# Optimization experiments

Measured on AMD Instinct MI355X. Metric: run time of the kernel, lower is better.

The kernel has to match this reference:

```python
import jax, jax.numpy as jnp
import numpy as np

B, L, HID, NH = 4, 1024, 768, 12
HD = HID // NH  # head dim 64
VOCAB, MPE = 30, 2048
NW, WL = 8, 16
BETA = 1.0


def setup_inputs() -> dict:
    key = jax.random.key(0)
    ks = jax.random.split(key, 10)
    hidden_states = jax.random.normal(ks[0], (B, L, HID), dtype=jnp.float32)
    attention_mask = jnp.zeros((B, 1, 1, L), dtype=jnp.float32)
    distance = jax.random.randint(ks[1], (B, L, L), 0, 1022, dtype=jnp.int32)
    random_walk = jax.random.randint(ks[2], (B, L, NW, WL), 0, VOCAB, dtype=jnp.int32)
    anonymous_random_walk = jax.random.randint(ks[3], (B, L, NW, WL), 0, VOCAB, dtype=jnp.int32)
    s = 0.02
    Wq = jax.random.normal(ks[4], (HID, HID), dtype=jnp.float32) * s
    Wk = jax.random.normal(ks[5], (HID, HID), dtype=jnp.float32) * s
    Wv = jax.random.normal(ks[6], (HID, HID), dtype=jnp.float32) * s
    bq = jnp.zeros((HID,), jnp.float32)
    bk = jnp.zeros((HID,), jnp.float32)
    bv = jnp.zeros((HID,), jnp.float32)
    node_emb = jax.random.normal(ks[7], (VOCAB, HID), dtype=jnp.float32) * s
    node_emb = node_emb.at[0].set(0.0)  # padding_idx=0
    dist_emb = jax.random.normal(ks[8], (MPE, NH), dtype=jnp.float32) * s
    dist_emb = dist_emb.at[0].set(0.0)  # padding_idx=0
    return dict(hidden_states=hidden_states, attention_mask=attention_mask,
                Wq=Wq, bq=bq, Wk=Wk, bk=bk, Wv=Wv, bv=bv,
                node_emb=node_emb, dist_emb=dist_emb,
                distance=distance, random_walk=random_walk,
                anonymous_random_walk=anonymous_random_walk)


def _heads(x):  # [B,L,HID] -> [B,NH,L,HD]
    return x.reshape(B, L, NH, HD).transpose(0, 2, 1, 3)


def _walk_bias(walk, node_emb):
    # walk: [B,L,NW,WL] int -> embed [B,L,NW,WL,HID] -> sum dims (2,3) -> [B,L,HID]
    pe = jnp.sum(node_emb[walk], axis=(2, 3))
    e = _heads(pe)  # [B,NH,L,HD]
    return jnp.einsum('bhid,bhjd->bhij', e, e)


def reference(hidden_states, attention_mask, Wq, bq, Wk, bk, Wv, bv,
              node_emb, dist_emb, distance, random_walk, anonymous_random_walk):
    q = _heads(hidden_states @ Wq.T + bq)
    k = _heads(hidden_states @ Wk.T + bk)
    v = _heads(hidden_states @ Wv.T + bv)
    scores = jnp.einsum('bhid,bhjd->bhij', q, k) / np.sqrt(HD).astype(np.float32)
    # distance RPE: [B,L,L,NH] -> [B,NH,L,L]
    bias = dist_emb[distance + 1].transpose(0, 3, 1, 2)
    bias = bias + _walk_bias(random_walk, node_emb)
    bias = bias + _walk_bias(anonymous_random_walk, node_emb)
    scores = scores + bias * BETA + attention_mask
    probs = jax.nn.softmax(scores, axis=-1)
    ctx = jnp.einsum('bhij,bhjd->bhid', probs, v)
    return ctx.transpose(0, 2, 1, 3).reshape(B, L, HID)
```

## Files before the change

### kernel.cpp

```cpp
#include <hip/hip_runtime.h>
#include <hip/hip_bf16.h>

#define LL 1024
#define HID 768
#define NH 12
#define HD 64
#define KAUG 192
#define NBH 48

typedef unsigned int u32;
typedef unsigned short u16;
typedef __bf16 bf16_t;
typedef bf16_t bf16x8 __attribute__((ext_vector_type(8)));
typedef _Float16 f16x4 __attribute__((ext_vector_type(4)));
typedef float f32x4 __attribute__((ext_vector_type(4)));
typedef u32 u32x4 __attribute__((ext_vector_type(4)));

__device__ __forceinline__ u16 f2b(float f) {
    union { float f; u32 u; } v; v.f = f;
    u32 r = v.u + 0x7fffu + ((v.u >> 16) & 1u);
    return (u16)(r >> 16);
}
__device__ __forceinline__ u16 f2h(float f) {
    _Float16 h = (_Float16)f;
    return __builtin_bit_cast(u16, h);
}
__device__ __forceinline__ float h2f(u16 v) {
    return (float)__builtin_bit_cast(_Float16, v);
}
__device__ __forceinline__ bf16x8 load8s(const u16* p) {
    return __builtin_bit_cast(bf16x8, *reinterpret_cast<const u32x4*>(p));
}
__device__ __forceinline__ f16x4 load4h(const u16* p) {
    return __builtin_bit_cast(f16x4, *reinterpret_cast<const unsigned long long*>(p));
}
__device__ __forceinline__ void cvt4_store_v(u16* dst, float4 f) {
    ushort4 o;
    o.x = f2b(f.x); o.y = f2b(f.y); o.z = f2b(f.z); o.w = f2b(f.w);
    *reinterpret_cast<ushort4*>(dst) = o;
}

__global__ __launch_bounds__(256) void k_pack(const int* __restrict__ distance, u16* __restrict__ distu) {
    int idx = (blockIdx.x * 256 + threadIdx.x) * 8;
    int4 a = *reinterpret_cast<const int4*>(&distance[idx]);
    int4 b = *reinterpret_cast<const int4*>(&distance[idx + 4]);
    u32x4 w;
    w[0] = (u32)(u16)(a.x + 1) | ((u32)(u16)(a.y + 1) << 16);
    w[1] = (u32)(u16)(a.z + 1) | ((u32)(u16)(a.w + 1) << 16);
    w[2] = (u32)(u16)(b.x + 1) | ((u32)(u16)(b.y + 1) << 16);
    w[3] = (u32)(u16)(b.z + 1) | ((u32)(u16)(b.w + 1) << 16);
    *reinterpret_cast<u32x4*>(&distu[idx]) = w;
}

__global__ __launch_bounds__(256) void k_qkv(const float* __restrict__ hs,
                                             const float* __restrict__ Wq, const float* __restrict__ Wk,
                                             const float* __restrict__ Wv,
                                             const float* __restrict__ bq, const float* __restrict__ bk,
                                             const float* __restrict__ bv,
                                             u16* __restrict__ Qa, u16* __restrict__ Ka,
                                             u16* __restrict__ Vt) {
    __shared__ __align__(16) u16 smem[18432];
    u16* a_s = smem;
    u16* b_s = smem + 9216;
    int m0 = blockIdx.x * 128;
    int nt = blockIdx.y;
    int which = nt / 6;
    int n0w = (nt % 6) * 128;
    const float* W    = (which == 0) ? Wq : (which == 1) ? Wk : Wv;
    const float* bias = (which == 0) ? bq : (which == 1) ? bk : bv;
    int tid = threadIdx.x;
    int wave = tid >> 6, lane = tid & 63, l15 = lane & 15, qd = lane >> 4;
    int wm = wave >> 1, wn = wave & 1;

    int srow = tid >> 4, scol = (tid & 15) * 4;

    f32x4 acc[4][4];
    for (int i = 0; i < 4; i++)
        for (int j = 0; j < 4; j++) acc[i][j] = f32x4{0.f, 0.f, 0.f, 0.f};

    float4 pa[8], pb[8];
#pragma unroll
    for (int it = 0; it < 8; it++) {
        int row = srow + it * 16;
        pa[it] = *reinterpret_cast<const float4*>(&hs[(size_t)(m0 + row) * 768 + scol]);
        pb[it] = *reinterpret_cast<const float4*>(&W[(size_t)(n0w + row) * 768 + scol]);
    }
    for (int k0 = 0; k0 < 768; k0 += 64) {
        __syncthreads();
#pragma unroll
        for (int it = 0; it < 8; it++) {
            int row = srow + it * 16;
            cvt4_store_v(&a_s[row * 72 + scol], pa[it]);
            cvt4_store_v(&b_s[row * 72 + scol], pb[it]);
        }
        __syncthreads();
        if (k0 < 704) {
            int k1 = k0 + 64;
#pragma unroll
            for (int it = 0; it < 8; it++) {
                int row = srow + it * 16;
                pa[it] = *reinterpret_cast<const float4*>(&hs[(size_t)(m0 + row) * 768 + k1 + scol]);
                pb[it] = *reinterpret_cast<const float4*>(&W[(size_t)(n0w + row) * 768 + k1 + scol]);
            }
        }
        for (int kk = 0; kk < 2; kk++) {
            bf16x8 af[4], bf[4];
            for (int i = 0; i < 4; i++) af[i] = load8s(&a_s[(wm * 64 + i * 16 + l15) * 72 + kk * 32 + qd * 8]);
            for (int j = 0; j < 4; j++) bf[j] = load8s(&b_s[(wn * 64 + j * 16 + l15) * 72 + kk * 32 + qd * 8]);
            for (int i = 0; i < 4; i++)
                for (int j = 0; j < 4; j++)
                    acc[i][j] = __builtin_amdgcn_mfma_f32_16x16x32_bf16(af[i], bf[j], acc[i][j], 0, 0, 0);
        }
    }
    __syncthreads();
    int b = m0 >> 10, l0b = m0 & 1023;
    if (which != 2) {
        float qscale = (which == 0) ? 0.125f : 1.0f;
        for (int i = 0; i < 4; i++) {
            int m_loc = wm * 64 + i * 16 + qd * 4;
            for (int j = 0; j < 4; j++) {
                int n_loc = wn * 64 + j * 16 + l15;
                float bv_ = bias[n0w + n_loc];
                for (int r = 0; r < 4; r++)
                    smem[(m_loc + r) * 136 + n_loc] = f2b((acc[i][j][r] + bv_) * qscale);
            }
        }
        __syncthreads();
        u16* dstbuf = (which == 0) ? Qa : Ka;
        for (int it = 0; it < 8; it++) {
            int c = tid + it * 256;
            int row = c >> 4, col = (c & 15) * 8;
            u32x4 w = *reinterpret_cast<u32x4*>(&smem[row * 136 + col]);
            int nn = n0w + col;
            int h = nn >> 6, d = nn & 63;
            size_t dst = ((size_t)(b * NH + h) * LL + (l0b + row)) * KAUG + d;
            *reinterpret_cast<u32x4*>(&dstbuf[dst]) = w;
        }
    } else {
        for (int i = 0; i < 4; i++) {
            int m_loc = wm * 64 + i * 16 + qd * 4;
            for (int j = 0; j < 4; j++) {
                int n_loc = wn * 64 + j * 16 + l15;
                float bv_ = bias[n0w + n_loc];
                for (int r = 0; r < 4; r++)
                    smem[n_loc * 136 + (m_loc + r)] = f2h(acc[i][j][r] + bv_);
            }
        }
        __syncthreads();
        for (int it = 0; it < 8; it++) {
            int c = tid + it * 256;
            int n = c >> 4, m_off = (c & 15) * 8;
            u32x4 w = *reinterpret_cast<u32x4*>(&smem[n * 136 + m_off]);
            int nn = n0w + n;
            int h = nn >> 6, d = nn & 63;
            size_t dst = ((size_t)(b * NH + h) * HD + d) * LL + (l0b + m_off);
            *reinterpret_cast<u32x4*>(&Vt[dst]) = w;
        }
    }
}

__global__ __launch_bounds__(256) void k_pe(const int* __restrict__ rw,
                                            const int* __restrict__ arw,
                                            const float* __restrict__ node_emb,
                                            u16* __restrict__ Qa, u16* __restrict__ Ka) {
    int m = blockIdx.x;
    __shared__ int hist[64];
    __shared__ float c1[32], c2[32];
    __shared__ __align__(16) u16 pe_s[12 * 128];
    int t = threadIdx.x;
    if (t < 64) hist[t] = 0;
    __syncthreads();
    if (t < 128) atomicAdd(&hist[rw[m * 128 + t] & 31], 1);
    else         atomicAdd(&hist[32 + (arw[m * 128 + (t - 128)] & 31)], 1);
    __syncthreads();
    if (t < 64) {
        if (t < 32) c1[t] = (float)hist[t];
        else        c2[t - 32] = (float)hist[t];
    }
    __syncthreads();
    for (int c = t; c < 768; c += 256) {
        float s1 = 0.f, s2 = 0.f;
        for (int v = 0; v < 30; v++) {
            float ne = node_emb[v * 768 + c];
            s1 += c1[v] * ne;
            s2 += c2[v] * ne;
        }
        int h = c >> 6, d = c & 63;
        pe_s[h * 128 + d]      = f2b(s1);
        pe_s[h * 128 + 64 + d] = f2b(s2);
    }
    __syncthreads();
    int b = m >> 10, l = m & 1023;
    if (t < 192) {
        int h = t >> 4, ch = t & 15;
        u32x4 w = *reinterpret_cast<const u32x4*>(&pe_s[h * 128 + ch * 8]);
        size_t dst = ((size_t)(b * NH + h) * LL + l) * KAUG + 64 + ch * 8;
        *reinterpret_cast<u32x4*>(&Qa[dst]) = w;
        *reinterpret_cast<u32x4*>(&Ka[dst]) = w;
    }
}

__global__ __launch_bounds__(256, 2) void k_attn(const u16* __restrict__ Qa, const u16* __restrict__ Ka,
                                                 const u16* __restrict__ Vt,
                                                 const u16* __restrict__ distu,
                                                 const float* __restrict__ dist_emb,
                                                 const float* __restrict__ mask,
                                                 u16* __restrict__ Opart,
                                                 float2* __restrict__ MLpart)
{
    __shared__ __align__(16) u16 ka_s[64][200];
    __shared__ __align__(16) u16 vt_s[64][80];
    __shared__ float distcol[2048];

    int bx = blockIdx.x;
    int jh = bx >> 3, ipair = bx & 7;
    int bh = blockIdx.y;
    int b = bh / NH, h = bh % NH;
    int tid = threadIdx.x, wave = tid >> 6, lane = tid & 63, l15 = lane & 15, qd = lane >> 4;

    const u16* Qh = Qa + (size_t)bh * LL * KAUG;
    const u16* Kh = Ka + (size_t)bh * LL * KAUG;
    const u16* Vh = Vt + (size_t)bh * HD * LL;
    const u16* distb = distu + (size_t)b * LL * LL;
    const float* maskb = mask + (size_t)b * LL;
    int jbase = jh * 512;

    for (int t = tid; t < 2048; t += 256) distcol[t] = dist_emb[t * NH + h];

    int i0A = ipair * 128 + wave * 16;
    int i0B = i0A + 64;
    bf16x8 aqA[6], aqB[6];
#pragma unroll
    for (int ks = 0; ks < 6; ks++) {
        aqA[ks] = load8s(&Qh[(size_t)(i0A + l15) * KAUG + ks * 32 + qd * 8]);
        aqB[ks] = load8s(&Qh[(size_t)(i0B + l15) * KAUG + ks * 32 + qd * 8]);
    }

    f32x4 oA[4], oB[4];
#pragma unroll
    for (int i = 0; i < 4; i++) { oA[i] = f32x4{0.f, 0.f, 0.f, 0.f}; oB[i] = f32x4{0.f, 0.f, 0.f, 0.f}; }
    float mA = -1e30f, lA = 0.f, mB = -1e30f, lB = 0.f;

    u32x4 kbuf[6], vbuf[2];
    ushort4 dpA[4], dpB[4];
#pragma unroll
    for (int it = 0; it < 6; it++) {
        int c = tid + it * 256;
        int row = c / 24, col = (c % 24) * 8;
        kbuf[it] = *reinterpret_cast<const u32x4*>(&Kh[(size_t)(jbase + row) * KAUG + col]);
    }
#pragma unroll
    for (int it = 0; it < 2; it++) {
        int c = tid + it * 256;
        int d = c >> 3, col = (c & 7) * 8;
        vbuf[it] = *reinterpret_cast<const u32x4*>(&Vh[(size_t)d * LL + jbase + col]);
    }
#pragma unroll
    for (int jf = 0; jf < 4; jf++) {
        dpA[jf] = *reinterpret_cast<const ushort4*>(&distb[(size_t)(i0A + l15) * LL + jbase + jf * 16 + qd * 4]);
        dpB[jf] = *reinterpret_cast<const ushort4*>(&distb[(size_t)(i0B + l15) * LL + jbase + jf * 16 + qd * 4]);
    }

    auto half = [&](const bf16x8* aq, ushort4* dp, f32x4* o, float& m_i, float& l_i,
                    const float4* mk, int i0, int j0n) {
        f32x4 st[4];
#pragma unroll
        for (int jf = 0; jf < 4; jf++) st[jf] = f32x4{0.f, 0.f, 0.f, 0.f};
        __builtin_amdgcn_s_setprio(1);
#pragma unroll
        for (int ks = 0; ks < 6; ks++) {
#pragma unroll
            for (int jf = 0; jf < 4; jf++) {
                bf16x8 ak = load8s(&ka_s[jf * 16 + l15][ks * 32 + qd * 8]);
                st[jf] = __builtin_amdgcn_mfma_f32_16x16x32_bf16(ak, aq[ks], st[jf], 0, 0, 0);
            }
        }
        __builtin_amdgcn_s_setprio(0);
#pragma unroll
        for (int jf = 0; jf < 4; jf++) {
            st[jf][0] += distcol[dp[jf].x] + mk[jf].x;
            st[jf][1] += distcol[dp[jf].y] + mk[jf].y;
            st[jf][2] += distcol[dp[jf].z] + mk[jf].z;
            st[jf][3] += distcol[dp[jf].w] + mk[jf].w;
        }
        if (j0n >= 0) {
#pragma unroll
            for (int jf = 0; jf < 4; jf++)
                dp[jf] = *reinterpret_cast<const ushort4*>(&distb[(size_t)(i0 + l15) * LL + j0n + jf * 16 + qd * 4]);
        }
        float m0_ = fmaxf(fmaxf(st[0][0], st[0][1]), fmaxf(st[0][2], st[0][3]));
        float m1_ = fmaxf(fmaxf(st[1][0], st[1][1]), fmaxf(st[1][2], st[1][3]));
        float m2_ = fmaxf(fmaxf(st[2][0], st[2][1]), fmaxf(st[2][2], st[2][3]));
        float m3_ = fmaxf(fmaxf(st[3][0], st[3][1]), fmaxf(st[3][2], st[3][3]));
        float mx = fmaxf(fmaxf(m0_, m1_), fmaxf(m2_, m3_));
        mx = fmaxf(mx, __shfl_xor(mx, 16));
        mx = fmaxf(mx, __shfl_xor(mx, 32));
        if (!__all(mx <= m_i + 8.0f)) {
            float mnew = fmaxf(m_i, mx);
            float alpha = __expf(m_i - mnew);
            m_i = mnew;
            l_i *= alpha;
            float a0 = __shfl(alpha, qd * 4 + 0, 16);
            float a1 = __shfl(alpha, qd * 4 + 1, 16);
            float a2 = __shfl(alpha, qd * 4 + 2, 16);
            float a3 = __shfl(alpha, qd * 4 + 3, 16);
#pragma unroll
            for (int df = 0; df < 4; df++) {
                o[df][0] *= a0; o[df][1] *= a1; o[df][2] *= a2; o[df][3] *= a3;
            }
        }
        float ssum = 0.f;
        f16x4 pf[4];
#pragma unroll
        for (int jf = 0; jf < 4; jf++) {
            float p0 = __expf(st[jf][0] - m_i);
            float p1 = __expf(st[jf][1] - m_i);
            float p2 = __expf(st[jf][2] - m_i);
            float p3 = __expf(st[jf][3] - m_i);
            ssum += (p0 + p1) + (p2 + p3);
            pf[jf] = f16x4{(_Float16)p0, (_Float16)p1, (_Float16)p2, (_Float16)p3};
        }
        ssum += __shfl_xor(ssum, 16);
        ssum += __shfl_xor(ssum, 32);
        l_i += ssum;
        __builtin_amdgcn_s_setprio(1);
#pragma unroll
        for (int jf = 0; jf < 4; jf++) {
#pragma unroll
            for (int df = 0; df < 4; df++) {
                f16x4 vf = load4h(&vt_s[df * 16 + l15][jf * 16 + qd * 4]);
                o[df] = __builtin_amdgcn_mfma_f32_16x16x16f16(pf[jf], vf, o[df], 0, 0, 0);
            }
        }
        __builtin_amdgcn_s_setprio(0);
    };

    for (int jt = 0; jt < 8; jt++) {
        int j0 = jbase + jt * 64;
        __syncthreads();
#pragma unroll
        for (int it = 0; it < 6; it++) {
            int c = tid + it * 256;
            int row = c / 24, col = (c % 24) * 8;
            *reinterpret_cast<u32x4*>(&ka_s[row][col]) = kbuf[it];
        }
#pragma unroll
        for (int it = 0; it < 2; it++) {
            int c = tid + it * 256;
            int d = c >> 3, col = (c & 7) * 8;
            *reinterpret_cast<u32x4*>(&vt_s[d][col]) = vbuf[it];
        }
        __syncthreads();
        if (jt < 7) {
            int j0n = j0 + 64;
#pragma unroll
            for (int it = 0; it < 6; it++) {
                int c = tid + it * 256;
                int row = c / 24, col = (c % 24) * 8;
                kbuf[it] = *reinterpret_cast<const u32x4*>(&Kh[(size_t)(j0n + row) * KAUG + col]);
            }
#pragma unroll
            for (int it = 0; it < 2; it++) {
                int c = tid + it * 256;
                int d = c >> 3, col = (c & 7) * 8;
                vbuf[it] = *reinterpret_cast<const u32x4*>(&Vh[(size_t)d * LL + j0n + col]);
            }
        }
        float4 mk[4];
#pragma unroll
        for (int jf = 0; jf < 4; jf++)
            mk[jf] = *reinterpret_cast<const float4*>(&maskb[j0 + jf * 16 + qd * 4]);
        int j0n = (jt < 7) ? j0 + 64 : -1;
        half(aqA, dpA, oA, mA, lA, mk, i0A, j0n);
        half(aqB, dpB, oB, mB, lB, mk, i0B, j0n);
    }

    __syncthreads();
    u16* ost = &ka_s[0][0] + wave * 16 * 72;
    u16* Oj = Opart + (size_t)jh * NBH * LL * HD;
    float2* MLj = MLpart + (size_t)jh * NBH * LL;
    auto epi = [&](const f32x4* o, float m_i, float l_i, int i0) {
        float lr0 = 1.f / __shfl(l_i, qd * 4 + 0, 16);
        float lr1 = 1.f / __shfl(l_i, qd * 4 + 1, 16);
        float lr2 = 1.f / __shfl(l_i, qd * 4 + 2, 16);
        float lr3 = 1.f / __shfl(l_i, qd * 4 + 3, 16);
#pragma unroll
        for (int df = 0; df < 4; df++) {
            int d = df * 16 + l15;
            ost[(qd * 4 + 0) * 72 + d] = f2h(o[df][0] * lr0);
            ost[(qd * 4 + 1) * 72 + d] = f2h(o[df][1] * lr1);
            ost[(qd * 4 + 2) * 72 + d] = f2h(o[df][2] * lr2);
            ost[(qd * 4 + 3) * 72 + d] = f2h(o[df][3] * lr3);
        }
#pragma unroll
        for (int it = 0; it < 2; it++) {
            int row = (lane >> 3) + it * 8;
            int ch = lane & 7;
            u32x4 w = *reinterpret_cast<const u32x4*>(&ost[row * 72 + ch * 8]);
            size_t base = (((size_t)bh << 10) + i0 + row) * HD + ch * 8;
            *reinterpret_cast<u32x4*>(&Oj[base]) = w;
        }
        if (qd == 0) MLj[((size_t)bh << 10) + i0 + l15] = float2{m_i, l_i};
    };
    epi(oA, mA, lA, i0A);
    __builtin_amdgcn_s_waitcnt(0);
    epi(oB, mB, lB, i0B);
}

__global__ __launch_bounds__(256) void k_comb(const u16* __restrict__ Opart,
                                              const float2* __restrict__ MLpart,
                                              void* __restrict__ outv, int f32mode) {
    int t = threadIdx.x;
    int row = blockIdx.x * 16 + (t >> 4);
    int dq = (t & 15) * 4;
    int bh = row >> 10, i = row & 1023;
    int b = bh / NH, h = bh % NH;
    const u16* O0 = Opart;
    const u16* O1 = Opart + (size_t)NBH * LL * HD;
    float2 a = MLpart[row];
    float2 c = MLpart[(size_t)NBH * LL + row];
    float M = fmaxf(a.x, c.x);
    float w0 = a.y * __expf(a.x - M), w1 = c.y * __expf(c.x - M);
    float inv = 1.f / (w0 + w1);
    float s0 = w0 * inv, s1 = w1 * inv;
    ushort4 o0 = *reinterpret_cast<const ushort4*>(&O0[((size_t)row) * HD + dq]);
    ushort4 o1 = *reinterpret_cast<const ushort4*>(&O1[((size_t)row) * HD + dq]);
    float v0 = h2f(o0.x) * s0 + h2f(o1.x) * s1;
    float v1 = h2f(o0.y) * s0 + h2f(o1.y) * s1;
    float v2 = h2f(o0.z) * s0 + h2f(o1.z) * s1;
    float v3 = h2f(o0.w) * s0 + h2f(o1.w) * s1;
    size_t idx = ((size_t)(b * LL + i)) * HID + h * 64 + dq;
    if (f32mode) {
        *reinterpret_cast<float4*>(&((float*)outv)[idx]) = float4{v0, v1, v2, v3};
    } else {
        ushort4 w;
        w.x = f2b(v0); w.y = f2b(v1); w.z = f2b(v2); w.w = f2b(v3);
        *reinterpret_cast<ushort4*>(&((u16*)outv)[idx]) = w;
    }
}

extern "C" void kernel_launch(void* const* d_in, const int* in_sizes, int n_in,
                              void* d_out, int out_size, void* d_ws, size_t ws_size,
                              hipStream_t stream) {
    const float* hs       = (const float*)d_in[0];
    const float* mask     = (const float*)d_in[1];
    const float* Wq       = (const float*)d_in[2];
    const float* bq       = (const float*)d_in[3];
    const float* Wk       = (const float*)d_in[4];
    const float* bk       = (const float*)d_in[5];
    const float* Wv       = (const float*)d_in[6];
    const float* bv       = (const float*)d_in[7];
    const float* node_emb = (const float*)d_in[8];
    const float* dist_emb = (const float*)d_in[9];
    const int* distance   = (const int*)d_in[10];
    const int* rw         = (const int*)d_in[11];
    const int* arw        = (const int*)d_in[12];

    int f32mode = 0;
    {
        hipDeviceptr_t base = nullptr; size_t sz = 0;
        if (hipMemGetAddressRange(&base, &sz, (hipDeviceptr_t)d_out) == hipSuccess) {
            size_t off = (size_t)((char*)d_out - (char*)base);
            if (sz - off >= (size_t)out_size * 4u) f32mode = 1;
        }
    }

    u16* Qa = (u16*)d_ws;
    u16* Ka = Qa + (size_t)NBH * LL * KAUG;
    u16* Vt = Ka + (size_t)NBH * LL * KAUG;
    u16* distu = Vt + (size_t)NBH * HD * LL;
    u16* Opart = distu + (size_t)4 * LL * LL;
    float2* MLpart = (float2*)(Opart + (size_t)2 * NBH * LL * HD);

    k_pack<<<dim3(2048), dim3(256), 0, stream>>>(distance, distu);
    k_qkv<<<dim3(32, 18), dim3(256), 0, stream>>>(hs, Wq, Wk, Wv, bq, bk, bv, Qa, Ka, Vt);
    k_pe<<<dim3(4096), dim3(256), 0, stream>>>(rw, arw, node_emb, Qa, Ka);
    k_attn<<<dim3(16, 48), dim3(256), 0, stream>>>(Qa, Ka, Vt, distu, dist_emb, mask, Opart, MLpart);
    k_comb<<<dim3(NBH * LL / 16), dim3(256), 0, stream>>>(Opart, MLpart, d_out, f32mode);
}
```

Measured before the change: 248.3 us.

## Pre-convert QKV GEMM inputs to bf16 and remap attention blocks per XCD

Adds two conversion kernels that turn hidden states and the three weight matrices into bf16 once, staging them in the Opart workspace region. The QKV GEMM then loads half as many bytes per tile and skips per-tile fp32-to-bf16 conversion. The attention kernel's block index is remapped so that all blocks of a given batch-head land on the same XCD, to improve L2 reuse of K/V. The cost is two extra kernel launches and an extra pass over the fp32 inputs.

```diff
diff --git a/kernel.cpp b/kernel.cpp
--- a/kernel.cpp
+++ b/kernel.cpp
@@ -38,6 +38,24 @@
     ushort4 o;
     o.x = f2b(f.x); o.y = f2b(f.y); o.z = f2b(f.z); o.w = f2b(f.w);
     *reinterpret_cast<ushort4*>(dst) = o;
+}
+
+__global__ __launch_bounds__(256) void k_cvt(const float* __restrict__ src, u16* __restrict__ dst) {
+    int idx = (blockIdx.x * 256 + threadIdx.x) * 8;
+    float4 a = *reinterpret_cast<const float4*>(&src[idx]);
+    float4 b = *reinterpret_cast<const float4*>(&src[idx + 4]);
+    cvt4_store_v(&dst[idx], a);
+    cvt4_store_v(&dst[idx + 4], b);
+}
+__global__ __launch_bounds__(256) void k_cvtw(const float* __restrict__ Wq, const float* __restrict__ Wk,
+                                              const float* __restrict__ Wv, u16* __restrict__ dst) {
+    const float* s = (blockIdx.y == 0) ? Wq : (blockIdx.y == 1) ? Wk : Wv;
+    int idx = (blockIdx.x * 256 + threadIdx.x) * 8;
+    float4 a = *reinterpret_cast<const float4*>(&s[idx]);
+    float4 b = *reinterpret_cast<const float4*>(&s[idx + 4]);
+    u16* d = dst + (size_t)blockIdx.y * 768 * 768;
+    cvt4_store_v(&d[idx], a);
+    cvt4_store_v(&d[idx + 4], b);
 }
 
 __global__ __launch_bounds__(256) void k_pack(const int* __restrict__ distance, u16* __restrict__ distu) {
@@ -52,9 +70,8 @@
     *reinterpret_cast<u32x4*>(&distu[idx]) = w;
 }
 
-__global__ __launch_bounds__(256) void k_qkv(const float* __restrict__ hs,
-                                             const float* __restrict__ Wq, const float* __restrict__ Wk,
-                                             const float* __restrict__ Wv,
+__global__ __launch_bounds__(256) void k_qkv(const u16* __restrict__ hs16,
+                                             const u16* __restrict__ w16,
                                              const float* __restrict__ bq, const float* __restrict__ bk,
                                              const float* __restrict__ bv,
                                              u16* __restrict__ Qa, u16* __restrict__ Ka,
@@ -66,41 +83,41 @@
     int nt = blockIdx.y;
     int which = nt / 6;
     int n0w = (nt % 6) * 128;
-    const float* W    = (which == 0) ? Wq : (which == 1) ? Wk : Wv;
+    const u16* W = w16 + (size_t)which * 768 * 768;
     const float* bias = (which == 0) ? bq : (which == 1) ? bk : bv;
     int tid = threadIdx.x;
     int wave = tid >> 6, lane = tid & 63, l15 = lane & 15, qd = lane >> 4;
     int wm = wave >> 1, wn = wave & 1;
 
-    int srow = tid >> 4, scol = (tid & 15) * 4;
+    int srow = tid >> 3, scol = (tid & 7) * 8;
 
     f32x4 acc[4][4];
     for (int i = 0; i < 4; i++)
         for (int j = 0; j < 4; j++) acc[i][j] = f32x4{0.f, 0.f, 0.f, 0.f};
 
-    float4 pa[8], pb[8];
-#pragma unroll
-    for (int it = 0; it < 8; it++) {
-        int row = srow + it * 16;
-        pa[it] = *reinterpret_cast<const float4*>(&hs[(size_t)(m0 + row) * 768 + scol]);
-        pb[it] = *reinterpret_cast<const float4*>(&W[(size_t)(n0w + row) * 768 + scol]);
+    u32x4 pa[4], pb[4];
+#pragma unroll
+    for (int it = 0; it < 4; it++) {
+        int row = srow + it * 32;
+        pa[it] = *reinterpret_cast<const u32x4*>(&hs16[(size_t)(m0 + row) * 768 + scol]);
+        pb[it] = *reinterpret_cast<const u32x4*>(&W[(size_t)(n0w + row) * 768 + scol]);
     }
     for (int k0 = 0; k0 < 768; k0 += 64) {
         __syncthreads();
 #pragma unroll
-        for (int it = 0; it < 8; it++) {
-            int row = srow + it * 16;
-            cvt4_store_v(&a_s[row * 72 + scol], pa[it]);
-            cvt4_store_v(&b_s[row * 72 + scol], pb[it]);
+        for (int it = 0; it < 4; it++) {
+            int row = srow + it * 32;
+            *reinterpret_cast<u32x4*>(&a_s[row * 72 + scol]) = pa[it];
+            *reinterpret_cast<u32x4*>(&b_s[row * 72 + scol]) = pb[it];
         }
         __syncthreads();
         if (k0 < 704) {
             int k1 = k0 + 64;
 #pragma unroll
-            for (int it = 0; it < 8; it++) {
-                int row = srow + it * 16;
-                pa[it] = *reinterpret_cast<const float4*>(&hs[(size_t)(m0 + row) * 768 + k1 + scol]);
-                pb[it] = *reinterpret_cast<const float4*>(&W[(size_t)(n0w + row) * 768 + k1 + scol]);
+            for (int it = 0; it < 4; it++) {
+                int row = srow + it * 32;
+                pa[it] = *reinterpret_cast<const u32x4*>(&hs16[(size_t)(m0 + row) * 768 + k1 + scol]);
+                pb[it] = *reinterpret_cast<const u32x4*>(&W[(size_t)(n0w + row) * 768 + k1 + scol]);
             }
         }
         for (int kk = 0; kk < 2; kk++) {
@@ -212,9 +229,11 @@
     __shared__ __align__(16) u16 vt_s[64][80];
     __shared__ float distcol[2048];
 
-    int bx = blockIdx.x;
+    int lin = blockIdx.x + (blockIdx.y << 4);
+    int xcd = lin & 7, slot = lin >> 3;
+    int bh = xcd * 6 + (slot >> 4);
+    int bx = slot & 15;
     int jh = bx >> 3, ipair = bx & 7;
-    int bh = blockIdx.y;
     int b = bh / NH, h = bh % NH;
     int tid = threadIdx.x, wave = tid >> 6, lane = tid & 63, l15 = lane & 15, qd = lane >> 4;
 
@@ -471,9 +490,13 @@
     u16* distu = Vt + (size_t)NBH * HD * LL;
     u16* Opart = distu + (size_t)4 * LL * LL;
     float2* MLpart = (float2*)(Opart + (size_t)2 * NBH * LL * HD);
-
+    u16* hs16 = Opart;
+    u16* w16  = Opart + (size_t)4096 * 768;
+
+    k_cvt<<<dim3(1536), dim3(256), 0, stream>>>(hs, hs16);
+    k_cvtw<<<dim3(288, 3), dim3(256), 0, stream>>>(Wq, Wk, Wv, w16);
     k_pack<<<dim3(2048), dim3(256), 0, stream>>>(distance, distu);
-    k_qkv<<<dim3(32, 18), dim3(256), 0, stream>>>(hs, Wq, Wk, Wv, bq, bk, bv, Qa, Ka, Vt);
+    k_qkv<<<dim3(32, 18), dim3(256), 0, stream>>>(hs16, w16, bq, bk, bv, Qa, Ka, Vt);
     k_pe<<<dim3(4096), dim3(256), 0, stream>>>(rw, arw, node_emb, Qa, Ka);
     k_attn<<<dim3(16, 48), dim3(256), 0, stream>>>(Qa, Ka, Vt, distu, dist_emb, mask, Opart, MLpart);
     k_comb<<<dim3(NBH * LL / 16), dim3(256), 0, stream>>>(Opart, MLpart, d_out, f32mode);
```

Result: faster. 229.5 us (-7.6%).
